# Kernel optimization log

Hardware: AMD Instinct MI355X
Metric: run time of the kernel (lower is better)

## Reference

```python
import jax, jax.numpy as jnp
import numpy as np
import math

DIM = 1024
MAX_DEPTH = 16
ROPE_BASE = 10000.0
NUM_ACTIVE = 2

def setup_inputs() -> dict:
    key = jax.random.key(0)
    ks = jax.random.split(key, 6)
    bsz, seq, dim, E, hidden = 4, 1024, DIM, 8, 4 * DIM
    bound = 1.0 / math.sqrt(dim)
    return {
        "x": jax.random.normal(ks[0], (bsz, seq, dim), jnp.float32),
        "router_w": jax.random.normal(ks[1], (dim, dim), jnp.float32) * 0.02,
        "expert_keys": jax.random.uniform(ks[2], (E, dim), jnp.float32, -bound, bound),
        "expert_bias": jnp.zeros((E,), jnp.float32),
        "fc_w": jax.random.normal(ks[3], (E, hidden, dim), jnp.float32) * 0.02,
        "proj_w": jax.random.normal(ks[4], (E, dim, hidden), jnp.float32) * 0.02,
        "depth_idx": 3,
    }

def _rope_row(depth_idx, rev_idx, dtype):
    half = DIM // 2
    inv_freq = 1.0 / (ROPE_BASE ** (jnp.arange(0, DIM, 2, dtype=jnp.float32) / DIM))  # [half]
    f = depth_idx * inv_freq
    r = rev_idx * inv_freq
    return (jnp.cos(f).astype(dtype), jnp.sin(f).astype(dtype),
            jnp.cos(r).astype(dtype), jnp.sin(r).astype(dtype))

def reference(x, router_w, expert_keys, expert_bias, fc_w, proj_w, depth_idx):
    bsz, seq, dim = x.shape
    N = bsz * seq
    flat_x = x.reshape(N, dim)
    # router + RMSNorm (no weight, eps = machine eps, matching F.rms_norm default)
    q = flat_x @ router_w.T
    eps = jnp.asarray(jnp.finfo(q.dtype).eps, q.dtype)
    q = q * jax.lax.rsqrt(jnp.mean(q * q, axis=-1, keepdims=True) + eps)
    # depth RoPE (forward freq on first half pairing, reverse freq on second half)
    half = dim // 2
    cos, sin, rcos, rsin = _rope_row(float(depth_idx), float(MAX_DEPTH - 1 - depth_idx), q.dtype)
    q1, q2 = q[..., :half], q[..., half:]
    q = jnp.concatenate((q1 * cos + q2 * sin, -q1 * rsin + q2 * rcos), axis=-1)
    # routing
    logits = (q @ expert_keys.T) / math.sqrt(dim)  # [N, E]
    gate_values = jax.nn.sigmoid(logits)
    biased = logits + expert_bias
    _, topk_idx = jax.lax.top_k(biased, NUM_ACTIVE)  # [N, k]
    topk_gates = jnp.take_along_axis(gate_values, topk_idx, axis=-1)
    topk_gates = topk_gates / jnp.clip(topk_gates.sum(-1, keepdims=True), 1e-9, None)
    gates = jnp.zeros_like(gate_values).at[jnp.arange(N)[:, None], topk_idx].set(topk_gates)
    # dense all-expert MLP: relu(x W_fc^T)^2 W_proj^T, then mask-and-sum
    h = jax.nn.relu(jnp.einsum('nd,ehd->neh', flat_x, fc_w))
    expert_out = jnp.einsum('neh,edh->ned', h * h, proj_w)  # [N, E, dim]
    y = jnp.einsum('ned,ne->nd', expert_out, gates)
    return y.reshape(bsz, seq, dim)
```

## Files before the change

kernel.cpp:

```cpp
#include <hip/hip_runtime.h>
#include <hip/hip_bf16.h>
#include <math.h>

#define N_TOK 4096
#define DIM_V 1024
#define NEXP  8
#define HID   4096
#define NSLOT 9216

typedef short  s16x8 __attribute__((ext_vector_type(8)));
typedef unsigned short u16x8 __attribute__((ext_vector_type(8)));
typedef float  f32x4 __attribute__((ext_vector_type(4)));

constexpr size_t OFF_XB   = 0;
constexpr size_t OFF_WB   = OFF_XB + 8388608;
constexpr size_t OFF_RK   = OFF_WB + 2097152;
constexpr size_t OFF_KPP  = OFF_RK + 65536;
constexpr size_t OFF_SSQ  = OFF_KPP + 65536;
constexpr size_t OFF_CNT  = OFF_SSQ + 16384;
constexpr size_t OFF_CUR  = OFF_CNT + 128;
constexpr size_t OFF_TOK  = OFF_CUR + 128;
constexpr size_t OFF_GSL  = OFF_TOK + 36864;
constexpr size_t ZERO_BEG = OFF_KPP;
constexpr size_t ZERO_END = OFF_GSL + 36864;
constexpr size_t OFF_OFFP = ZERO_END;
constexpr size_t OFF_IDX2 = OFF_OFFP + 128;
constexpr size_t OFF_G2   = OFF_IDX2 + 32768;
constexpr size_t OFF_INV  = OFF_G2 + 32768;
constexpr size_t SMALL_END = OFF_INV + 32768;

constexpr size_t A_OFF_FCB = SMALL_END;
constexpr size_t A_OFF_PO  = A_OFF_FCB;
constexpr size_t A_OFF_PJB = A_OFF_FCB + 67108864;
constexpr size_t A_OFF_H2  = A_OFF_PJB + 67108864;
constexpr size_t WS_FULL   = A_OFF_H2 + 75497472;

__device__ inline unsigned short f2bf(float f) {
  __hip_bfloat16 h = __float2bfloat16(f);
  return __builtin_bit_cast(unsigned short, h);
}

__device__ __forceinline__ void gload16(const void* g, void* l) {
  __builtin_amdgcn_global_load_lds(
      (const __attribute__((address_space(1))) unsigned int*)g,
      (__attribute__((address_space(3))) unsigned int*)l, 16, 0, 0);
}

__global__ void k_cvt_all(const float* __restrict__ x, const float* __restrict__ rw,
                          const float* __restrict__ fw, const float* __restrict__ pw,
                          unsigned short* __restrict__ xb, unsigned short* __restrict__ wb,
                          unsigned short* __restrict__ fcb, unsigned short* __restrict__ pjb) {
  const int NX = (N_TOK * DIM_V) / 8, NW = (DIM_V * DIM_V) / 8;
  const int NF = (NEXP * HID * DIM_V) / 8;
  const int total = NX + NW + NF + NF;
  for (int i = blockIdx.x * blockDim.x + threadIdx.x; i < total;
       i += gridDim.x * blockDim.x) {
    const float* s; unsigned short* d; int j;
    if (i < NX)                { s = x;  d = xb;  j = i; }
    else if (i < NX + NW)      { s = rw; d = wb;  j = i - NX; }
    else if (i < NX + NW + NF) { s = fw; d = fcb; j = i - NX - NW; }
    else                       { s = pw; d = pjb; j = i - NX - NW - NF; }
    float4 a = ((const float4*)s)[2 * j];
    float4 b = ((const float4*)s)[2 * j + 1];
    u16x8 o = { f2bf(a.x), f2bf(a.y), f2bf(a.z), f2bf(a.w),
                f2bf(b.x), f2bf(b.y), f2bf(b.z), f2bf(b.w) };
    *(u16x8*)(d + (size_t)j * 8) = o;
  }
}

__global__ void k_ropekeys(const float* __restrict__ keys, const int* __restrict__ depth,
                           double* __restrict__ rk) {
  int i = threadIdx.x;
  if (i >= 512) return;
  int dep = depth[0];
  double p = pow(10000.0, (double)i / 512.0);
  float invf = 1.0f / (float)p;
  float ff = (float)dep * invf;
  float rr = (float)(15 - dep) * invf;
  float cf  = (float)cos((double)ff);
  float sf  = (float)sin((double)ff);
  float rcf = (float)cos((double)rr);
  float rsf = (float)sin((double)rr);
  for (int e = 0; e < NEXP; ++e) {
    double k1 = (double)keys[e * DIM_V + i];
    double k2 = (double)keys[e * DIM_V + 512 + i];
    rk[e * DIM_V + i]       = (double)cf  * k1 - (double)rsf * k2;
    rk[e * DIM_V + 512 + i] = (double)sf  * k1 + (double)rcf * k2;
  }
}

__global__ __launch_bounds__(256) void k_colsum(const float* __restrict__ W,
                                                const double* __restrict__ rk,
                                                double* __restrict__ kpp) {
  int j  = blockIdx.x * 256 + threadIdx.x;
  int d0 = blockIdx.y * 64;
  double acc[NEXP] = {};
  for (int dd = 0; dd < 64; ++dd) {
    int d = d0 + dd;
    double w = (double)W[(size_t)d * DIM_V + j];
#pragma unroll
    for (int e = 0; e < NEXP; ++e) acc[e] += w * rk[e * DIM_V + d];
  }
  for (int e = 0; e < NEXP; ++e) atomicAdd(&kpp[e * DIM_V + j], acc[e]);
}

__global__ __launch_bounds__(256) void k_gate(const float* __restrict__ x,
                                              const double* __restrict__ kpp,
                                              const float* __restrict__ sumsq,
                                              const float* __restrict__ bias,
                                              int* __restrict__ idx2, float* __restrict__ gates2,
                                              int* __restrict__ counts) {
  int wave = (blockIdx.x * 256 + threadIdx.x) >> 6;
  int lane = threadIdx.x & 63;
  if (wave >= N_TOK) return;
  const float4* xr = (const float4*)(x + (size_t)wave * DIM_V);
  double a[NEXP] = {};
#pragma unroll
  for (int j = 0; j < 4; ++j) {
    int c = lane + 64 * j;
    float4 v = xr[c];
#pragma unroll
    for (int e = 0; e < NEXP; ++e) {
      const double* kp = kpp + (size_t)e * DIM_V + c * 4;
      a[e] += (double)v.x * kp[0] + (double)v.y * kp[1] +
              (double)v.z * kp[2] + (double)v.w * kp[3];
    }
  }
#pragma unroll
  for (int e = 0; e < NEXP; ++e)
    for (int d = 1; d < 64; d <<= 1) a[e] += __shfl_xor(a[e], d, 64);
  if (lane == 0) {
    float s = rsqrtf(sumsq[wave] * (1.0f / 1024.0f) + 1.1920928955078125e-7f);
    float z[NEXP], b[NEXP];
#pragma unroll
    for (int e = 0; e < NEXP; ++e) {
      z[e] = (float)(a[e] * (double)s * (1.0 / 32.0));
      b[e] = z[e] + bias[e];
    }
    int i1 = 0;
    for (int e = 1; e < NEXP; ++e) if (b[e] > b[i1]) i1 = e;
    int i2 = -1;
    for (int e = 0; e < NEXP; ++e) if (e != i1 && (i2 < 0 || b[e] > b[i2])) i2 = e;
    float g1 = 1.f / (1.f + expf(-z[i1]));
    float g2 = 1.f / (1.f + expf(-z[i2]));
    float sm = fmaxf(g1 + g2, 1e-9f);
    idx2[wave * 2] = i1; idx2[wave * 2 + 1] = i2;
    gates2[wave * 2] = g1 / sm; gates2[wave * 2 + 1] = g2 / sm;
    atomicAdd(&counts[i1], 1); atomicAdd(&counts[i2], 1);
  }
}

__global__ void k_scatter(const int* __restrict__ idx2, const float* __restrict__ gates2,
                          const int* __restrict__ counts, int* __restrict__ cursor,
                          int* __restrict__ tok, float* __restrict__ gsl,
                          int* __restrict__ inv, int* __restrict__ offp_out) {
  int off[NEXP + 1];
  off[0] = 0;
  for (int e = 0; e < NEXP; ++e) off[e + 1] = off[e] + ((counts[e] + 127) & ~127);
  int n = blockIdx.x * 256 + threadIdx.x;
  if (blockIdx.x == 0 && threadIdx.x == 0)
    for (int e = 0; e <= NEXP; ++e) offp_out[e] = off[e];
  if (n >= N_TOK) return;
  for (int r = 0; r < 2; ++r) {
    int e = idx2[n * 2 + r];
    int pos = atomicAdd(&cursor[e], 1);
    int slot = off[e] + pos;
    tok[slot] = n; gsl[slot] = gates2[n * 2 + r]; inv[n * 2 + r] = slot;
  }
}

__global__ __launch_bounds__(512) void k_fc256(
    const unsigned short* __restrict__ xb,
    const unsigned short* __restrict__ fcb,
    const int* __restrict__ offp, const int* __restrict__ tok,
    unsigned short* __restrict__ h2) {
  constexpr int KD = DIM_V;
  constexpr int NT = KD / 64;
  const int G = gridDim.x, q = G >> 3;
  const int idp = ((int)blockIdx.x & 7) * q + ((int)blockIdx.x >> 3);
  const int bx = idp >> 4;
  const int n0 = (idp & 15) * 256;
  int c = 0, e = 0, m0 = -1;
  for (e = 0; e < NEXP; ++e) {
    int nb = (offp[e + 1] - offp[e] + 255) >> 8;
    if (bx < c + nb) { m0 = offp[e] + (bx - c) * 256; break; }
    c += nb;
  }
  if (m0 < 0) return;
  const int segend = offp[e + 1];
  const unsigned short* Bp = fcb + ((size_t)e * HID + n0) * KD;

  __shared__ alignas(16) char smem[131072];
  const int tid = threadIdx.x, wid = tid >> 6, lane = tid & 63;
  const int wr = (wid >> 2) * 128, wcc = (wid & 3) * 64;
  const int swc8 = ((tid & 7) ^ ((tid >> 3) & 7)) * 8;
  const int frow = lane & 15, fsl = lane >> 4, fkey = lane & 7;

  int arow[4];
#pragma unroll
  for (int p = 0; p < 4; ++p) {
    int rr = m0 + p * 64 + (tid >> 3);
    arow[p] = tok[rr < NSLOT ? rr : NSLOT - 1];
  }

  auto stage = [&](int k0s, unsigned db) {
#pragma unroll
    for (int p = 0; p < 4; ++p)
      gload16(xb + (size_t)arow[p] * KD + k0s + swc8,
              smem + db + p * 8192 + wid * 1024);
#pragma unroll
    for (int p = 0; p < 4; ++p)
      gload16(Bp + (size_t)(p * 64 + (tid >> 3)) * KD + k0s + swc8,
              smem + db + 32768 + p * 8192 + wid * 1024);
  };

  f32x4 acc[8][4] = {};
  stage(0, 0);
  for (int t = 0; t < NT; ++t) {
    int tn = t + 1; if (tn == NT) tn = 0;
    stage(tn * 64, (unsigned)((t + 1) & 1) * 65536u);
    asm volatile("s_waitcnt vmcnt(8)" ::: "memory");
    __builtin_amdgcn_s_barrier();
    __builtin_amdgcn_sched_barrier(0);
    const unsigned Ab = (unsigned)(t & 1) * 65536u, Bb = Ab + 32768u;
#pragma unroll
    for (int kk2 = 0; kk2 < 2; ++kk2) {
      const unsigned so = (unsigned)(((fsl + kk2 * 4) ^ fkey) << 4);
      s16x8 af[8], bfr[4];
#pragma unroll
      for (int m = 0; m < 8; ++m)
        af[m] = *(const s16x8*)(smem + Ab + (unsigned)(wr + m * 16 + frow) * 128 + so);
#pragma unroll
      for (int n = 0; n < 4; ++n)
        bfr[n] = *(const s16x8*)(smem + Bb + (unsigned)(wcc + n * 16 + frow) * 128 + so);
      __builtin_amdgcn_s_setprio(1);
#pragma unroll
      for (int m = 0; m < 8; ++m)
#pragma unroll
        for (int n = 0; n < 4; ++n)
          acc[m][n] = __builtin_amdgcn_mfma_f32_16x16x32_bf16(af[m], bfr[n], acc[m][n], 0, 0, 0);
      __builtin_amdgcn_s_setprio(0);
    }
    __builtin_amdgcn_sched_barrier(0);
    __builtin_amdgcn_s_barrier();
  }
#pragma unroll
  for (int m = 0; m < 8; ++m)
#pragma unroll
    for (int j = 0; j < 4; ++j) {
      const int grow = m0 + wr + m * 16 + (lane >> 4) * 4 + j;
      if (grow < segend) {
#pragma unroll
        for (int n = 0; n < 4; ++n) {
          float v = acc[m][n][j];
          v = v > 0.f ? v * v : 0.f;
          h2[(size_t)grow * HID + n0 + wcc + n * 16 + (lane & 15)] = f2bf(v);
        }
      }
    }
}

template<int KD, int ONB, int EPI>
__global__ __launch_bounds__(256) void k_gemm(
    const unsigned short* __restrict__ Aptr,
    const unsigned short* __restrict__ Wptr,
    const int* __restrict__ offp,
    const float* __restrict__ gsl, void* __restrict__ outp) {
  constexpr int GNB = ONB / 128;
  constexpr int NT  = KD / 64;
  const int G = gridDim.x, q = G >> 3;
  const int idp = ((int)blockIdx.x & 7) * q + ((int)blockIdx.x >> 3);
  const int n0 = (idp % GNB) * 128, m0 = (idp / GNB) * 128;
  int e = 0;
  if constexpr (EPI == 1) {
    if (m0 >= offp[NEXP]) return;
    while (e < NEXP - 1 && m0 >= offp[e + 1]) ++e;
  }
  const unsigned short* Bp = Wptr + ((size_t)e * ONB + n0) * KD;

  __shared__ alignas(16) char smem[65536];
  const int tid = threadIdx.x, wid = tid >> 6, lane = tid & 63;
  const int wr = (wid >> 1) * 64, wc = (wid & 1) * 64;
  const int rql  = tid >> 3;
  const int swc8 = ((tid & 7) ^ ((tid >> 3) & 7)) * 8;
  const int frow = lane & 15, fsl = lane >> 4, fkey = lane & 7;

  auto stage = [&](int k0s, unsigned db) {
#pragma unroll
    for (int p = 0; p < 4; ++p)
      gload16(Aptr + (size_t)(m0 + p * 32 + rql) * KD + k0s + swc8,
              smem + db + p * 4096 + wid * 1024);
#pragma unroll
    for (int p = 0; p < 4; ++p)
      gload16(Bp + (size_t)(p * 32 + rql) * KD + k0s + swc8,
              smem + db + 16384 + p * 4096 + wid * 1024);
  };

  f32x4 acc[4][4] = {};
  stage(0, 0);
#pragma unroll 2
  for (int t = 0; t < NT; ++t) {
    int tn = t + 1; if (tn == NT) tn = 0;
    stage(tn * 64, (unsigned)((t + 1) & 1) * 32768u);
    asm volatile("s_waitcnt vmcnt(8)" ::: "memory");
    __builtin_amdgcn_s_barrier();
    __builtin_amdgcn_sched_barrier(0);
    const unsigned Ab = (unsigned)(t & 1) * 32768u, Bb = Ab + 16384u;
    s16x8 af[2][4], bfr[2][4];
#pragma unroll
    for (int kk2 = 0; kk2 < 2; ++kk2) {
      const unsigned so = (unsigned)(((fsl + kk2 * 4) ^ fkey) << 4);
#pragma unroll
      for (int m = 0; m < 4; ++m)
        af[kk2][m] = *(const s16x8*)(smem + Ab + (unsigned)(wr + m * 16 + frow) * 128 + so);
#pragma unroll
      for (int n = 0; n < 4; ++n)
        bfr[kk2][n] = *(const s16x8*)(smem + Bb + (unsigned)(wc + n * 16 + frow) * 128 + so);
    }
    __builtin_amdgcn_s_setprio(1);
#pragma unroll
    for (int kk2 = 0; kk2 < 2; ++kk2)
#pragma unroll
      for (int m = 0; m < 4; ++m)
#pragma unroll
        for (int n = 0; n < 4; ++n)
          acc[m][n] = __builtin_amdgcn_mfma_f32_16x16x32_bf16(af[kk2][m], bfr[kk2][n],
                                                              acc[m][n], 0, 0, 0);
    __builtin_amdgcn_s_setprio(0);
    __builtin_amdgcn_sched_barrier(0);
    __builtin_amdgcn_s_barrier();
  }

#pragma unroll
  for (int m = 0; m < 4; ++m)
#pragma unroll
    for (int j = 0; j < 4; ++j) {
      const int grow = m0 + wr + m * 16 + (lane >> 4) * 4 + j;
      if constexpr (EPI == 0) {
        float s = 0.f;
#pragma unroll
        for (int n = 0; n < 4; ++n) { float v = acc[m][n][j]; s += v * v; }
        s += __shfl_xor(s, 1, 64); s += __shfl_xor(s, 2, 64);
        s += __shfl_xor(s, 4, 64); s += __shfl_xor(s, 8, 64);
        if ((lane & 15) == 0) atomicAdd(&((float*)outp)[grow], s);
      } else {
        float* out = (float*)outp;
        const float g = gsl[grow];
#pragma unroll
        for (int n = 0; n < 4; ++n)
          out[(size_t)grow * ONB + n0 + wc + n * 16 + (lane & 15)] = acc[m][n][j] * g;
      }
    }
}

__global__ void k_combine(const float* __restrict__ po, const int* __restrict__ inv,
                          float* __restrict__ y) {
  const int total = N_TOK * (DIM_V / 4);
  for (int i = blockIdx.x * blockDim.x + threadIdx.x; i < total;
       i += gridDim.x * blockDim.x) {
    int n = i >> 8, c = i & 255;
    int s1 = inv[n * 2], s2 = inv[n * 2 + 1];
    float4 a = ((const float4*)(po + (size_t)s1 * DIM_V))[c];
    float4 b = ((const float4*)(po + (size_t)s2 * DIM_V))[c];
    float4 o; o.x = a.x + b.x; o.y = a.y + b.y; o.z = a.z + b.z; o.w = a.w + b.w;
    ((float4*)(y + (size_t)n * DIM_V))[c] = o;
  }
}

extern "C" void kernel_launch(void* const* d_in, const int* in_sizes, int n_in,
                              void* d_out, int out_size, void* d_ws, size_t ws_size,
                              hipStream_t stream) {
  if (ws_size < WS_FULL) return;
  const float* x      = (const float*)d_in[0];
  const float* rw     = (const float*)d_in[1];
  const float* keys   = (const float*)d_in[2];
  const float* bias   = (const float*)d_in[3];
  const float* fc_w   = (const float*)d_in[4];
  const float* proj_w = (const float*)d_in[5];
  const int*   depth  = (const int*)d_in[6];
  char* ws = (char*)d_ws;
  unsigned short* xb  = (unsigned short*)(ws + OFF_XB);
  unsigned short* wb  = (unsigned short*)(ws + OFF_WB);
  double* rk    = (double*)(ws + OFF_RK);
  double* kpp   = (double*)(ws + OFF_KPP);
  float*  ssq   = (float*)(ws + OFF_SSQ);
  int*    cnt   = (int*)(ws + OFF_CNT);
  int*    cur   = (int*)(ws + OFF_CUR);
  int*    tok   = (int*)(ws + OFF_TOK);
  float*  gsl   = (float*)(ws + OFF_GSL);
  int*    offp  = (int*)(ws + OFF_OFFP);
  int*    idx2  = (int*)(ws + OFF_IDX2);
  float*  g2    = (float*)(ws + OFF_G2);
  int*    inv   = (int*)(ws + OFF_INV);
  unsigned short* fcb = (unsigned short*)(ws + A_OFF_FCB);
  unsigned short* pjb = (unsigned short*)(ws + A_OFF_PJB);
  unsigned short* h2  = (unsigned short*)(ws + A_OFF_H2);
  float*  po    = (float*)(ws + A_OFF_PO);
  float*  y     = (float*)d_out;

  hipMemsetAsync(ws + ZERO_BEG, 0, ZERO_END - ZERO_BEG, stream);
  k_cvt_all<<<2048, 256, 0, stream>>>(x, rw, fc_w, proj_w, xb, wb, fcb, pjb);
  k_ropekeys<<<1, 512, 0, stream>>>(keys, depth, rk);
  k_colsum<<<dim3(4, 16), 256, 0, stream>>>(rw, rk, kpp);
  k_gemm<DIM_V, DIM_V, 0><<<dim3(32 * 8), 256, 0, stream>>>(xb, wb, offp, gsl, ssq);
  k_gate<<<1024, 256, 0, stream>>>(x, kpp, ssq, bias, idx2, g2, cnt);
  k_scatter<<<16, 256, 0, stream>>>(idx2, g2, cnt, cur, tok, gsl, inv, offp);
  k_fc256<<<dim3(44 * 16), 512, 0, stream>>>(xb, fcb, offp, tok, h2);
  k_gemm<HID, DIM_V, 1><<<dim3(72 * 8), 256, 0, stream>>>(h2, pjb, offp, gsl, po);
  k_combine<<<2048, 256, 0, stream>>>(po, inv, y);
}
```

Before: 473.8 us.

## Add per-expert 256x64 tiled proj GEMM and contiguous-chunk conversion kernel

Replaces the generic 128x128 grouped projection GEMM with a dedicated kernel. It uses 256-row by 64-column tiles with 512 threads, and its row blocks are aligned to each expert's segment instead of the padded global layout. This is meant to cut wasted tiles at expert boundaries and raise parallelism (704 blocks), at the cost of less B reuse per tile. The fp32-to-bf16 conversion kernel also changes from a grid-stride loop to contiguous per-block chunks with float4 granularity. The query GEMM is specialized into its own kernel with no functional change.

```diff
diff --git a/kernel.cpp b/kernel.cpp
--- a/kernel.cpp
+++ b/kernel.cpp
@@ -46,25 +46,33 @@
       (__attribute__((address_space(3))) unsigned int*)l, 16, 0, 0);
 }
 
-__global__ void k_cvt_all(const float* __restrict__ x, const float* __restrict__ rw,
-                          const float* __restrict__ fw, const float* __restrict__ pw,
-                          unsigned short* __restrict__ xb, unsigned short* __restrict__ wb,
-                          unsigned short* __restrict__ fcb, unsigned short* __restrict__ pjb) {
-  const int NX = (N_TOK * DIM_V) / 8, NW = (DIM_V * DIM_V) / 8;
-  const int NF = (NEXP * HID * DIM_V) / 8;
-  const int total = NX + NW + NF + NF;
-  for (int i = blockIdx.x * blockDim.x + threadIdx.x; i < total;
-       i += gridDim.x * blockDim.x) {
-    const float* s; unsigned short* d; int j;
-    if (i < NX)                { s = x;  d = xb;  j = i; }
-    else if (i < NX + NW)      { s = rw; d = wb;  j = i - NX; }
-    else if (i < NX + NW + NF) { s = fw; d = fcb; j = i - NX - NW; }
-    else                       { s = pw; d = pjb; j = i - NX - NW - NF; }
-    float4 a = ((const float4*)s)[2 * j];
-    float4 b = ((const float4*)s)[2 * j + 1];
-    u16x8 o = { f2bf(a.x), f2bf(a.y), f2bf(a.z), f2bf(a.w),
-                f2bf(b.x), f2bf(b.y), f2bf(b.z), f2bf(b.w) };
-    *(u16x8*)(d + (size_t)j * 8) = o;
+__global__ __launch_bounds__(256) void k_cvt_all(
+    const float* __restrict__ x, const float* __restrict__ rw,
+    const float* __restrict__ fw, const float* __restrict__ pw,
+    unsigned short* __restrict__ xb, unsigned short* __restrict__ wb,
+    unsigned short* __restrict__ fcb, unsigned short* __restrict__ pjb) {
+  constexpr int NX = (N_TOK * DIM_V) / 4;
+  constexpr int NW = (DIM_V * DIM_V) / 4;
+  constexpr int NF = (NEXP * HID * DIM_V) / 4;
+  const int cb[5] = {0, NX, NX + NW, NX + NW + NF, NX + NW + 2 * NF};
+  const float* sp[4] = {x, rw, fw, pw};
+  unsigned short* dp[4] = {xb, wb, fcb, pjb};
+  const int total = cb[4];
+  const int per = (total + (int)gridDim.x - 1) / (int)gridDim.x;
+  const int beg = (int)blockIdx.x * per;
+  const int end = (beg + per < total) ? beg + per : total;
+#pragma unroll
+  for (int r = 0; r < 4; ++r) {
+    int rb = beg > cb[r] ? beg : cb[r];
+    int re = end < cb[r + 1] ? end : cb[r + 1];
+    const float4* s = (const float4*)sp[r];
+    unsigned short* d = dp[r];
+    for (int i = rb + (int)threadIdx.x; i < re; i += 256) {
+      int j = i - cb[r];
+      float4 v = s[j];
+      ushort4 o = { f2bf(v.x), f2bf(v.y), f2bf(v.z), f2bf(v.w) };
+      *(ushort4*)(d + (size_t)j * 4) = o;
+    }
   }
 }
 
@@ -260,23 +268,104 @@
     }
 }
 
-template<int KD, int ONB, int EPI>
-__global__ __launch_bounds__(256) void k_gemm(
+__global__ __launch_bounds__(512) void k_proj256(
+    const unsigned short* __restrict__ h2,
+    const unsigned short* __restrict__ pjb,
+    const int* __restrict__ offp, const float* __restrict__ gsl,
+    float* __restrict__ po) {
+  constexpr int KD = HID;
+  constexpr int NT = KD / 64;
+  const int G = gridDim.x, q = G >> 3;
+  const int idp = ((int)blockIdx.x & 7) * q + ((int)blockIdx.x >> 3);
+  const int bx = idp >> 4;
+  const int n0 = (idp & 15) * 64;
+  int c = 0, e = 0, m0 = -1;
+  for (e = 0; e < NEXP; ++e) {
+    int nb = (offp[e + 1] - offp[e] + 255) >> 8;
+    if (bx < c + nb) { m0 = offp[e] + (bx - c) * 256; break; }
+    c += nb;
+  }
+  if (m0 < 0) return;
+  const int segend = offp[e + 1];
+  const unsigned short* Bp = pjb + ((size_t)e * DIM_V + n0) * KD;
+
+  __shared__ alignas(16) char smem[81920];
+  const int tid = threadIdx.x, wid = tid >> 6, lane = tid & 63;
+  const int wr = (wid >> 1) * 64, wc = (wid & 1) * 32;
+  const int swc8 = ((tid & 7) ^ ((tid >> 3) & 7)) * 8;
+  const int frow = lane & 15, fsl = lane >> 4, fkey = lane & 7;
+
+  int arow[4];
+#pragma unroll
+  for (int p = 0; p < 4; ++p) {
+    int rr = m0 + p * 64 + (tid >> 3);
+    arow[p] = rr < NSLOT ? rr : NSLOT - 1;
+  }
+
+  auto stage = [&](int k0s, unsigned db) {
+#pragma unroll
+    for (int p = 0; p < 4; ++p)
+      gload16(h2 + (size_t)arow[p] * KD + k0s + swc8,
+              smem + db + p * 8192 + wid * 1024);
+    gload16(Bp + (size_t)(tid >> 3) * KD + k0s + swc8,
+            smem + db + 32768 + wid * 1024);
+  };
+
+  f32x4 acc[4][2] = {};
+  stage(0, 0);
+  for (int t = 0; t < NT; ++t) {
+    int tn = t + 1; if (tn == NT) tn = 0;
+    stage(tn * 64, (unsigned)((t + 1) & 1) * 40960u);
+    asm volatile("s_waitcnt vmcnt(5)" ::: "memory");
+    __builtin_amdgcn_s_barrier();
+    __builtin_amdgcn_sched_barrier(0);
+    const unsigned Ab = (unsigned)(t & 1) * 40960u, Bb = Ab + 32768u;
+#pragma unroll
+    for (int kk2 = 0; kk2 < 2; ++kk2) {
+      const unsigned so = (unsigned)(((fsl + kk2 * 4) ^ fkey) << 4);
+      s16x8 af[4], bfr[2];
+#pragma unroll
+      for (int m = 0; m < 4; ++m)
+        af[m] = *(const s16x8*)(smem + Ab + (unsigned)(wr + m * 16 + frow) * 128 + so);
+#pragma unroll
+      for (int n = 0; n < 2; ++n)
+        bfr[n] = *(const s16x8*)(smem + Bb + (unsigned)(wc + n * 16 + frow) * 128 + so);
+      __builtin_amdgcn_s_setprio(1);
+#pragma unroll
+      for (int m = 0; m < 4; ++m)
+#pragma unroll
+        for (int n = 0; n < 2; ++n)
+          acc[m][n] = __builtin_amdgcn_mfma_f32_16x16x32_bf16(af[m], bfr[n], acc[m][n], 0, 0, 0);
+      __builtin_amdgcn_s_setprio(0);
+    }
+    __builtin_amdgcn_sched_barrier(0);
+    __builtin_amdgcn_s_barrier();
+  }
+#pragma unroll
+  for (int m = 0; m < 4; ++m)
+#pragma unroll
+    for (int j = 0; j < 4; ++j) {
+      const int grow = m0 + wr + m * 16 + (lane >> 4) * 4 + j;
+      if (grow < segend) {
+        const float g = gsl[grow];
+#pragma unroll
+        for (int n = 0; n < 2; ++n)
+          po[(size_t)grow * DIM_V + n0 + wc + n * 16 + (lane & 15)] = acc[m][n][j] * g;
+      }
+    }
+}
+
+__global__ __launch_bounds__(256) void k_qt(
     const unsigned short* __restrict__ Aptr,
     const unsigned short* __restrict__ Wptr,
-    const int* __restrict__ offp,
-    const float* __restrict__ gsl, void* __restrict__ outp) {
-  constexpr int GNB = ONB / 128;
+    float* __restrict__ sumsq) {
+  constexpr int KD = DIM_V;
+  constexpr int GNB = DIM_V / 128;
   constexpr int NT  = KD / 64;
   const int G = gridDim.x, q = G >> 3;
   const int idp = ((int)blockIdx.x & 7) * q + ((int)blockIdx.x >> 3);
   const int n0 = (idp % GNB) * 128, m0 = (idp / GNB) * 128;
-  int e = 0;
-  if constexpr (EPI == 1) {
-    if (m0 >= offp[NEXP]) return;
-    while (e < NEXP - 1 && m0 >= offp[e + 1]) ++e;
-  }
-  const unsigned short* Bp = Wptr + ((size_t)e * ONB + n0) * KD;
+  const unsigned short* Bp = Wptr + (size_t)n0 * KD;
 
   __shared__ alignas(16) char smem[65536];
   const int tid = threadIdx.x, wid = tid >> 6, lane = tid & 63;
@@ -336,20 +425,12 @@
 #pragma unroll
     for (int j = 0; j < 4; ++j) {
       const int grow = m0 + wr + m * 16 + (lane >> 4) * 4 + j;
-      if constexpr (EPI == 0) {
-        float s = 0.f;
-#pragma unroll
-        for (int n = 0; n < 4; ++n) { float v = acc[m][n][j]; s += v * v; }
-        s += __shfl_xor(s, 1, 64); s += __shfl_xor(s, 2, 64);
-        s += __shfl_xor(s, 4, 64); s += __shfl_xor(s, 8, 64);
-        if ((lane & 15) == 0) atomicAdd(&((float*)outp)[grow], s);
-      } else {
-        float* out = (float*)outp;
-        const float g = gsl[grow];
-#pragma unroll
-        for (int n = 0; n < 4; ++n)
-          out[(size_t)grow * ONB + n0 + wc + n * 16 + (lane & 15)] = acc[m][n][j] * g;
-      }
+      float s = 0.f;
+#pragma unroll
+      for (int n = 0; n < 4; ++n) { float v = acc[m][n][j]; s += v * v; }
+      s += __shfl_xor(s, 1, 64); s += __shfl_xor(s, 2, 64);
+      s += __shfl_xor(s, 4, 64); s += __shfl_xor(s, 8, 64);
+      if ((lane & 15) == 0) atomicAdd(&sumsq[grow], s);
     }
 }
 
@@ -402,10 +483,10 @@
   k_cvt_all<<<2048, 256, 0, stream>>>(x, rw, fc_w, proj_w, xb, wb, fcb, pjb);
   k_ropekeys<<<1, 512, 0, stream>>>(keys, depth, rk);
   k_colsum<<<dim3(4, 16), 256, 0, stream>>>(rw, rk, kpp);
-  k_gemm<DIM_V, DIM_V, 0><<<dim3(32 * 8), 256, 0, stream>>>(xb, wb, offp, gsl, ssq);
+  k_qt<<<dim3(32 * 8), 256, 0, stream>>>(xb, wb, ssq);
   k_gate<<<1024, 256, 0, stream>>>(x, kpp, ssq, bias, idx2, g2, cnt);
   k_scatter<<<16, 256, 0, stream>>>(idx2, g2, cnt, cur, tok, gsl, inv, offp);
   k_fc256<<<dim3(44 * 16), 512, 0, stream>>>(xb, fcb, offp, tok, h2);
-  k_gemm<HID, DIM_V, 1><<<dim3(72 * 8), 256, 0, stream>>>(h2, pjb, offp, gsl, po);
+  k_proj256<<<dim3(44 * 16), 512, 0, stream>>>(h2, pjb, offp, gsl, po);
   k_combine<<<2048, 256, 0, stream>>>(po, inv, y);
 }
```

New measurement: 483.1 us. About the same (+2.0%).
